# Optimization experiments

Measured on AMD Instinct MI355X. Metric: run time of the kernel, lower is better.

## Reference

```python
import math
import jax, jax.numpy as jnp
import numpy as np

N = 256                      # 'n' from __init__
LMAX = 15
NSH = (LMAX + 1) ** 2        # number of SH coefficients = 256
A = 2 * N                    # alpha grid size
B = N - 4                    # beta grid size (linspace(0,pi,n)[2:-2])
K = 1024                     # fixed max number of peaks per projection (jit-compatible capacity)
THR = 2.0 * math.pi / N      # dedup distance threshold


def _rot_zyz(a, b, c):
    def rz(t):
        return np.array([[math.cos(t), -math.sin(t), 0.0],
                         [math.sin(t),  math.cos(t), 0.0],
                         [0.0, 0.0, 1.0]])
    def ry(t):
        return np.array([[math.cos(t), 0.0, math.sin(t)],
                         [0.0, 1.0, 0.0],
                         [-math.sin(t), 0.0, math.cos(t)]])
    return rz(a) @ ry(b) @ rz(c)


def _grid_xyz(R):
    a = np.linspace(0.0, 2.0 * math.pi, A)
    b = np.linspace(0.0, math.pi, N)[2:-2]
    AA, BB = np.meshgrid(a, b, indexing='ij')       # [A, B]
    xyz = np.stack([np.sin(BB) * np.cos(AA),
                    np.sin(BB) * np.sin(AA),
                    np.cos(BB)], axis=-1)            # [A, B, 3]
    return (xyz @ R.T).astype(np.float32)


def setup_inputs() -> dict:
    key = jax.random.key(0)
    k1, k2, k3 = jax.random.split(key, 3)
    signal = jax.random.normal(k1, (NSH,), dtype=jnp.float32)
    # Precomputed SH projection buffers (fixed tensors in the torch module);
    # random stand-ins preserve the exact compute pattern of the einsum.
    sh1 = jax.random.normal(k2, (NSH, A, B), dtype=jnp.float32) * 0.1
    sh2 = jax.random.normal(k3, (NSH, A, B), dtype=jnp.float32) * 0.1
    xyz1 = jnp.asarray(_grid_xyz(_rot_zyz(math.pi / 2, math.pi / 2, math.pi / 2)))
    xyz2 = jnp.asarray(_grid_xyz(np.eye(3)))
    return {"signal": signal, "sh1": sh1, "sh2": sh2, "xyz1": xyz1, "xyz2": xyz2}


def _detect_peaks(signal, sh, xyz):
    # f[a,b] = sum_i signal[i] * sh[i,a,b]   (memory-bound GEMV over the grid)
    f = jnp.einsum('i,iab->ab', signal, sh)                       # [A, B]
    # strict local maxima along beta (rows) and alpha (columns); interior only
    row = jnp.pad((f[:, 1:-1] > f[:, :-2]) & (f[:, 1:-1] > f[:, 2:]),
                  ((0, 0), (1, 1)))
    col = jnp.pad((f[1:-1, :] > f[:-2, :]) & (f[1:-1, :] > f[2:, :]),
                  ((1, 1), (0, 0)))
    mask = (row & col).reshape(-1)                                # [A*B]
    ff = f.reshape(-1)
    score = jnp.where(mask, ff, -jnp.inf)
    _, idx = jax.lax.top_k(score, K)                              # fixed-capacity peak set
    valid = jnp.take(mask, idx)
    radius = jnp.where(valid, jnp.take(ff, idx), 0.0)             # [K]
    peaks = jnp.where(valid[:, None],
                      jnp.take(xyz.reshape(-1, 3), idx, axis=0), 0.0)  # [K, 3]
    return peaks, radius, valid


def reference(signal, sh1, sh2, xyz1, xyz2):
    p1, r1, v1 = _detect_peaks(signal, sh1, xyz1)
    p2, r2, v2 = _detect_peaks(signal, sh2, xyz2)
    # suppress peaks1 that lie within THR of any valid peak2
    d = jnp.linalg.norm(p1[:, None, :] - p2[None, :, :], axis=-1)  # [K, K]
    close = (d < THR) & v1[:, None] & v2[None, :]
    keep1 = v1 & ~jnp.any(close, axis=1)
    peaks = jnp.concatenate([jnp.where(keep1[:, None], p1, 0.0), p2], axis=0)   # [2K, 3]
    radius = jnp.concatenate([jnp.where(keep1, r1, 0.0), r2], axis=0)           # [2K]
    valid = jnp.concatenate([keep1, v2], axis=0)                                 # [2K]
    return peaks, radius, valid
```

## Files before the change

kernel.cpp:

```cpp
#include <hip/hip_runtime.h>
#include <hip/hip_bf16.h>
#include <stdint.h>

#define NSH 256
#define AG 512
#define BG 252
#define AB (AG*BG)
#define KK 1024
#define SENT 0xFFFFFFFFFFFFFFFFull

static __device__ __forceinline__ unsigned int fkey(float v){
    unsigned int u = __float_as_uint(v);
    u ^= (u >> 31) ? 0xFFFFFFFFu : 0x80000000u;
    return u;
}

__global__ __launch_bounds__(256) void k_gemv(const float* __restrict__ sig,
        const float* __restrict__ sh1, const float* __restrict__ sh2,
        float* __restrict__ f){
    __shared__ float s[NSH];
    s[threadIdx.x] = sig[threadIdx.x];
    __syncthreads();
    int proj = blockIdx.y;
    const float* sh = proj ? sh2 : sh1;
    int j = blockIdx.x * 256 + threadIdx.x;
    const float* p = sh + j;
    float a = 0.f;
    #pragma unroll 16
    for (int i = 0; i < NSH; ++i)
        a = fmaf(s[i], p[(size_t)i * AB], a);
    f[(size_t)proj * AB + j] = a;
}

__global__ __launch_bounds__(256) void k_mask(const float* __restrict__ f,
        unsigned long long* __restrict__ cand, unsigned int* __restrict__ counts){
    int proj = blockIdx.y;
    const float* fp = f + (size_t)proj * AB;
    int j = blockIdx.x * 256 + threadIdx.x;
    bool pred = false;
    unsigned long long key = 0;
    {
        int a = j / BG, b = j - a * BG;
        if (a > 0 && a < AG - 1 && b > 0 && b < BG - 1){
            float v = fp[j];
            pred = (v > fp[j-1]) && (v > fp[j+1]) && (v > fp[j-BG]) && (v > fp[j+BG]);
            if (pred)
                key = (((unsigned long long)(~fkey(v))) << 32) | (unsigned int)j;
        }
    }
    unsigned long long bal = __ballot(pred);
    if (bal){
        int lane = threadIdx.x & 63;
        int leader = __ffsll(bal) - 1;
        unsigned int base = 0;
        if (lane == leader) base = atomicAdd(&counts[proj], (unsigned int)__popcll(bal));
        base = __shfl(base, leader);
        if (pred){
            unsigned int off = (unsigned int)__popcll(bal & ((1ull << lane) - 1ull));
            cand[(size_t)proj * AB + base + off] = key;
        }
    }
}

__global__ __launch_bounds__(1024) void k_select(const unsigned long long* __restrict__ cand,
        const unsigned int* __restrict__ counts, unsigned long long* __restrict__ sel){
    int proj = blockIdx.y;
    const unsigned long long* cp = cand + (size_t)proj * AB;
    unsigned long long* sp = sel + proj * KK;
    unsigned int count = counts[proj];
    int tid = threadIdx.x;
    if (count <= KK){
        if (tid < KK) sp[tid] = SENT;
        if (tid < (int)count) sp[tid] = cp[tid];
        return;
    }
    __shared__ unsigned int hist[256];
    __shared__ unsigned int sbin, sremk;
    unsigned long long prefix = 0, pmask = 0;
    unsigned int remk = KK;
    for (int lvl = 7; lvl >= 0; --lvl){
        int shft = lvl * 8;
        if (tid < 256) hist[tid] = 0;
        __syncthreads();
        for (unsigned int i = tid; i < count; i += 1024){
            unsigned long long k = cp[i];
            if ((k & pmask) == prefix)
                atomicAdd(&hist[(unsigned int)(k >> shft) & 255u], 1u);
        }
        __syncthreads();
        if (tid < 64){
            unsigned int b0 = hist[tid*4+0], b1 = hist[tid*4+1];
            unsigned int b2 = hist[tid*4+2], b3 = hist[tid*4+3];
            unsigned int lsum = b0 + b1 + b2 + b3;
            unsigned int incl = lsum;
            #pragma unroll
            for (int off = 1; off < 64; off <<= 1){
                unsigned int v = __shfl_up(incl, off);
                if (tid >= off) incl += v;
            }
            unsigned int excl = incl - lsum;
            if (excl < remk && remk <= incl){
                unsigned int r = remk - excl;
                unsigned int c0 = b0, c01 = b0 + b1, c012 = b0 + b1 + b2;
                unsigned int bin, rr;
                if (r <= c0){ bin = tid*4+0; rr = r; }
                else if (r <= c01){ bin = tid*4+1; rr = r - c0; }
                else if (r <= c012){ bin = tid*4+2; rr = r - c01; }
                else { bin = tid*4+3; rr = r - c012; }
                sbin = bin; sremk = rr;
            }
        }
        __syncthreads();
        prefix |= ((unsigned long long)sbin) << shft;
        pmask  |= 0xFFull << shft;
        remk = sremk;
        __syncthreads();
    }
    __shared__ unsigned int pos;
    if (tid == 0) pos = 0;
    __syncthreads();
    for (unsigned int i = tid; i < count; i += 1024){
        unsigned long long k = cp[i];
        if (k <= prefix){
            unsigned int p = atomicAdd(&pos, 1u);
            sp[p] = k;
        }
    }
}

__global__ __launch_bounds__(1024) void k_sortgather(const unsigned long long* __restrict__ sel,
        const float* __restrict__ f, const float* __restrict__ xyz1,
        const float* __restrict__ xyz2, float4* __restrict__ pr,
        unsigned int* __restrict__ vb, float* __restrict__ out){
    int proj = blockIdx.y;
    int tid = threadIdx.x;
    __shared__ unsigned long long s[KK];
    s[tid] = sel[proj * KK + tid];
    __syncthreads();
    for (int k = 2; k <= KK; k <<= 1){
        for (int j = k >> 1; j > 0; j >>= 1){
            int ixj = tid ^ j;
            if (ixj > tid){
                unsigned long long a = s[tid], b = s[ixj];
                bool asc = (tid & k) == 0;
                if ((a > b) == asc){ s[tid] = b; s[ixj] = a; }
            }
            __syncthreads();
        }
    }
    unsigned long long key = s[tid];
    bool val = (key != SENT);
    unsigned int j = (unsigned int)key;
    const float* fp = f + (size_t)proj * AB;
    const float* xyz = proj ? xyz2 : xyz1;
    float4 o = make_float4(0.f, 0.f, 0.f, 0.f);
    if (val){
        o.x = xyz[(size_t)j * 3 + 0];
        o.y = xyz[(size_t)j * 3 + 1];
        o.z = xyz[(size_t)j * 3 + 2];
        o.w = fp[j];
    }
    pr[proj * KK + tid] = o;
    vb[proj * KK + tid] = val ? 1u : 0u;
    if (proj == 1){
        int row = KK + tid;
        out[row * 3 + 0] = o.x;
        out[row * 3 + 1] = o.y;
        out[row * 3 + 2] = o.z;
        out[2 * KK * 3 + row] = o.w;
        out[2 * KK * 3 + 2 * KK + row] = val ? 1.0f : 0.0f;
    }
}

__global__ __launch_bounds__(256) void k_dedup_mask(const float4* __restrict__ pr,
        const unsigned int* __restrict__ vb, unsigned int* __restrict__ suppress){
    const float THRF = (float)(6.283185307179586 / 256.0);
    int tid = threadIdx.x;
    __shared__ float sx[256], sy[256], sz[256];
    {
        int j = blockIdx.y * 256 + tid;
        float4 t = pr[KK + j];
        bool v2 = vb[KK + j] != 0;
        sx[tid] = v2 ? t.x : 1e9f;
        sy[tid] = v2 ? t.y : 1e9f;
        sz[tid] = v2 ? t.z : 1e9f;
    }
    __syncthreads();
    int k = blockIdx.x * 256 + tid;
    float4 m = pr[k];
    bool close = false;
    {
        #pragma clang fp contract(off)
        #pragma unroll 8
        for (int jj = 0; jj < 256; ++jj){
            float dx = m.x - sx[jj];
            float dy = m.y - sy[jj];
            float dz = m.z - sz[jj];
            float d2 = dx * dx + dy * dy + dz * dz;
            close = close | (sqrtf(d2) < THRF);
        }
    }
    if (close) atomicOr(&suppress[k], 1u);
}

__global__ __launch_bounds__(256) void k_out1(const float4* __restrict__ pr,
        const unsigned int* __restrict__ vb, const unsigned int* __restrict__ suppress,
        float* __restrict__ out){
    int k = blockIdx.x * 256 + threadIdx.x;
    float4 m = pr[k];
    bool keep = (vb[k] != 0) && (suppress[k] == 0);
    out[k * 3 + 0] = keep ? m.x : 0.0f;
    out[k * 3 + 1] = keep ? m.y : 0.0f;
    out[k * 3 + 2] = keep ? m.z : 0.0f;
    out[2 * KK * 3 + k] = keep ? m.w : 0.0f;
    out[2 * KK * 3 + 2 * KK + k] = keep ? 1.0f : 0.0f;
}

extern "C" void kernel_launch(void* const* d_in, const int* in_sizes, int n_in,
                              void* d_out, int out_size, void* d_ws, size_t ws_size,
                              hipStream_t stream){
    const float* sig  = (const float*)d_in[0];
    const float* sh1  = (const float*)d_in[1];
    const float* sh2  = (const float*)d_in[2];
    const float* xyz1 = (const float*)d_in[3];
    const float* xyz2 = (const float*)d_in[4];
    float* out = (float*)d_out;
    char* ws = (char*)d_ws;

    float* f                  = (float*)(ws);
    unsigned long long* cand  = (unsigned long long*)(ws + 0x100000);
    unsigned int* counts      = (unsigned int*)(ws + 0x300000);
    unsigned long long* sel   = (unsigned long long*)(ws + 0x300100);
    float4* pr                = (float4*)(ws + 0x310000);
    unsigned int* vb          = (unsigned int*)(ws + 0x320000);
    unsigned int* suppress    = (unsigned int*)(ws + 0x328000);

    (void)hipMemsetAsync(counts, 0, 2 * sizeof(unsigned int), stream);
    (void)hipMemsetAsync(suppress, 0, KK * sizeof(unsigned int), stream);

    k_gemv<<<dim3(AB / 256, 2), dim3(256), 0, stream>>>(sig, sh1, sh2, f);
    k_mask<<<dim3(AB / 256, 2), dim3(256), 0, stream>>>(f, cand, counts);
    k_select<<<dim3(1, 2), dim3(1024), 0, stream>>>(cand, counts, sel);
    k_sortgather<<<dim3(1, 2), dim3(1024), 0, stream>>>(sel, f, xyz1, xyz2, pr, vb, out);
    k_dedup_mask<<<dim3(4, 4), dim3(256), 0, stream>>>(pr, vb, suppress);
    k_out1<<<dim3(4, 1), dim3(256), 0, stream>>>(pr, vb, suppress, out);
}
```

Baseline: 180.9 us.

## Vectorize GEMV with float4 double-buffered loads and fuse dedup with output

The GEMV now has each thread compute four adjacent grid points, using float4 loads that are double-buffered in registers eight rows deep. This raises memory-level parallelism on the bandwidth-bound 256x129k read. The counts reset moves into the GEMV kernel and both memsets are removed. The dedup mask and the output kernel are merged into one kernel that loops over all 1024 peak2 entries per block, which removes the atomics and a launch. The cost is fewer GEMV blocks, higher register pressure and a longer serial loop per dedup thread.

```diff
diff --git a/kernel.cpp b/kernel.cpp
--- a/kernel.cpp
+++ b/kernel.cpp
@@ -17,19 +17,49 @@
 
 __global__ __launch_bounds__(256) void k_gemv(const float* __restrict__ sig,
         const float* __restrict__ sh1, const float* __restrict__ sh2,
-        float* __restrict__ f){
-    __shared__ float s[NSH];
-    s[threadIdx.x] = sig[threadIdx.x];
-    __syncthreads();
+        float* __restrict__ f, unsigned int* __restrict__ counts){
+    if (blockIdx.x == 0 && blockIdx.y == 0 && threadIdx.x < 2)
+        counts[threadIdx.x] = 0;
     int proj = blockIdx.y;
     const float* sh = proj ? sh2 : sh1;
-    int j = blockIdx.x * 256 + threadIdx.x;
-    const float* p = sh + j;
-    float a = 0.f;
-    #pragma unroll 16
-    for (int i = 0; i < NSH; ++i)
-        a = fmaf(s[i], p[(size_t)i * AB], a);
-    f[(size_t)proj * AB + j] = a;
+    size_t j4 = ((size_t)blockIdx.x * 256 + threadIdx.x) * 4;
+    const float* p = sh + j4;
+    float a0 = 0.f, a1 = 0.f, a2 = 0.f, a3 = 0.f;
+    float4 bufA[8], bufB[8];
+    #pragma unroll
+    for (int u = 0; u < 8; ++u)
+        bufA[u] = *reinterpret_cast<const float4*>(p + (size_t)u * AB);
+    #pragma unroll
+    for (int ii = 0; ii < NSH; ii += 16){
+        #pragma unroll
+        for (int u = 0; u < 8; ++u){
+            int nx = ii + 8 + u;
+            if (nx < NSH) bufB[u] = *reinterpret_cast<const float4*>(p + (size_t)nx * AB);
+        }
+        #pragma unroll
+        for (int u = 0; u < 8; ++u){
+            float si = sig[ii + u];
+            a0 = fmaf(si, bufA[u].x, a0);
+            a1 = fmaf(si, bufA[u].y, a1);
+            a2 = fmaf(si, bufA[u].z, a2);
+            a3 = fmaf(si, bufA[u].w, a3);
+        }
+        #pragma unroll
+        for (int u = 0; u < 8; ++u){
+            int nx = ii + 16 + u;
+            if (nx < NSH) bufA[u] = *reinterpret_cast<const float4*>(p + (size_t)nx * AB);
+        }
+        #pragma unroll
+        for (int u = 0; u < 8; ++u){
+            float si = sig[ii + 8 + u];
+            a0 = fmaf(si, bufB[u].x, a0);
+            a1 = fmaf(si, bufB[u].y, a1);
+            a2 = fmaf(si, bufB[u].z, a2);
+            a3 = fmaf(si, bufB[u].w, a3);
+        }
+    }
+    float4 o; o.x = a0; o.y = a1; o.z = a2; o.w = a3;
+    *reinterpret_cast<float4*>(f + (size_t)proj * AB + j4) = o;
 }
 
 __global__ __launch_bounds__(256) void k_mask(const float* __restrict__ f,
@@ -172,18 +202,19 @@
     }
 }
 
-__global__ __launch_bounds__(256) void k_dedup_mask(const float4* __restrict__ pr,
-        const unsigned int* __restrict__ vb, unsigned int* __restrict__ suppress){
+__global__ __launch_bounds__(256) void k_dedup(const float4* __restrict__ pr,
+        const unsigned int* __restrict__ vb, float* __restrict__ out){
     const float THRF = (float)(6.283185307179586 / 256.0);
     int tid = threadIdx.x;
-    __shared__ float sx[256], sy[256], sz[256];
-    {
-        int j = blockIdx.y * 256 + tid;
-        float4 t = pr[KK + j];
-        bool v2 = vb[KK + j] != 0;
-        sx[tid] = v2 ? t.x : 1e9f;
-        sy[tid] = v2 ? t.y : 1e9f;
-        sz[tid] = v2 ? t.z : 1e9f;
+    __shared__ float sx[KK], sy[KK], sz[KK];
+    #pragma unroll
+    for (int t = 0; t < 4; ++t){
+        int idx = t * 256 + tid;
+        float4 v = pr[KK + idx];
+        bool v2 = vb[KK + idx] != 0;
+        sx[idx] = v2 ? v.x : 1e9f;
+        sy[idx] = v2 ? v.y : 1e9f;
+        sz[idx] = v2 ? v.z : 1e9f;
     }
     __syncthreads();
     int k = blockIdx.x * 256 + tid;
@@ -192,7 +223,7 @@
     {
         #pragma clang fp contract(off)
         #pragma unroll 8
-        for (int jj = 0; jj < 256; ++jj){
+        for (int jj = 0; jj < KK; ++jj){
             float dx = m.x - sx[jj];
             float dy = m.y - sy[jj];
             float dz = m.z - sz[jj];
@@ -200,15 +231,7 @@
             close = close | (sqrtf(d2) < THRF);
         }
     }
-    if (close) atomicOr(&suppress[k], 1u);
-}
-
-__global__ __launch_bounds__(256) void k_out1(const float4* __restrict__ pr,
-        const unsigned int* __restrict__ vb, const unsigned int* __restrict__ suppress,
-        float* __restrict__ out){
-    int k = blockIdx.x * 256 + threadIdx.x;
-    float4 m = pr[k];
-    bool keep = (vb[k] != 0) && (suppress[k] == 0);
+    bool keep = (vb[k] != 0) && !close;
     out[k * 3 + 0] = keep ? m.x : 0.0f;
     out[k * 3 + 1] = keep ? m.y : 0.0f;
     out[k * 3 + 2] = keep ? m.z : 0.0f;
@@ -233,15 +256,10 @@
     unsigned long long* sel   = (unsigned long long*)(ws + 0x300100);
     float4* pr                = (float4*)(ws + 0x310000);
     unsigned int* vb          = (unsigned int*)(ws + 0x320000);
-    unsigned int* suppress    = (unsigned int*)(ws + 0x328000);
-
-    (void)hipMemsetAsync(counts, 0, 2 * sizeof(unsigned int), stream);
-    (void)hipMemsetAsync(suppress, 0, KK * sizeof(unsigned int), stream);
-
-    k_gemv<<<dim3(AB / 256, 2), dim3(256), 0, stream>>>(sig, sh1, sh2, f);
+
+    k_gemv<<<dim3(AB / 1024, 2), dim3(256), 0, stream>>>(sig, sh1, sh2, f, counts);
     k_mask<<<dim3(AB / 256, 2), dim3(256), 0, stream>>>(f, cand, counts);
     k_select<<<dim3(1, 2), dim3(1024), 0, stream>>>(cand, counts, sel);
     k_sortgather<<<dim3(1, 2), dim3(1024), 0, stream>>>(sel, f, xyz1, xyz2, pr, vb, out);
-    k_dedup_mask<<<dim3(4, 4), dim3(256), 0, stream>>>(pr, vb, suppress);
-    k_out1<<<dim3(4, 1), dim3(256), 0, stream>>>(pr, vb, suppress, out);
-}
+    k_dedup<<<dim3(4, 1), dim3(256), 0, stream>>>(pr, vb, out);
+}
```

Measured after the change: 213.2 us. 1.18x slower.
